# Performance work log

Measured on AMD Instinct MI355X. Metric: run time of the kernel, lower is better.

## Reference

```python
import jax, jax.numpy as jnp
import numpy as np

NUM_HEADS = 4
WINDOW_SIZE = 7
DILATION = 1


def local_mask(height, width, window_size, dilation):
    """[N, N] bool mask: True where token i may attend to token j (dilated 2D window)."""
    radius = window_size // 2
    rows = jnp.arange(height)
    cols = jnp.arange(width)
    r = jnp.repeat(rows, width)          # [N] row index of each flattened token
    c = jnp.tile(cols, height)           # [N] col index of each flattened token
    dr = r[:, None] - r[None, :]         # [N, N]
    dc = c[:, None] - c[None, :]
    within = (jnp.abs(dr) <= radius * dilation) & (jnpp_abs(dc) <= radius * dilation) if False else (
        (jnp.abs(dr) <= radius * dilation) & (jnp.abs(dc) <= radius * dilation)
    )
    on_grid = (dr % dilation == 0) & (dc % dilation == 0)
    return within & on_grid


def setup_inputs() -> dict:
    key = jax.random.key(0)
    kq, kk, kv = jax.random.split(key, 3)
    shape = (2, 64, 64, 64)  # (B, C, H, W)
    q = jax.random.normal(kq, shape, dtype=jnp.float32)
    k = jax.random.normal(kk, shape, dtype=jnp.float32)
    v = jax.random.normal(kv, shape, dtype=jnp.float32)
    return {"q": q, "k": k, "v": v}


def reference(q, k, v):
    B, C, H, W = q.shape
    nh = NUM_HEADS
    hd = C // nh
    N = H * W

    def to_seq(x):
        # (B, C, H, W) -> (B, nh, N, hd)
        x = x.reshape(B, nh, hd, H, W)
        return x.transpose(0, 1, 3, 4, 2).reshape(B, nh, N, hd)

    q_seq = to_seq(q)
    k_seq = to_seq(k)
    v_seq = to_seq(v)

    scale = 1.0 / jnp.sqrt(jnp.asarray(hd, dtype=q.dtype))
    scores = jnp.einsum("bhqd,bhkd->bhqk", q_seq, k_seq) * scale  # [B, nh, N, N]

    mask = local_mask(H, W, WINDOW_SIZE, DILATION)  # [N, N] bool
    neg = jnp.finfo(scores.dtype).min
    scores = jnp.where(mask[None, None, :, :], scores, neg)

    attn = jax.nn.softmax(scores, axis=-1)
    out = jnp.einsum("bhqk,bhkd->bhqd", attn, v_seq)  # [B, nh, N, hd]

    # (B, nh, N, hd) -> (B, C, H, W)
    out = out.reshape(B, nh, H, W, hd).transpose(0, 1, 4, 2, 3).reshape(B, C, H, W)
    return out
```

## Files before the change

kernel.cpp:

```cpp
#include <hip/hip_runtime.h>
#include <hip/hip_bf16.h>
#include <math.h>

#define HD  16
#define HW  4096
#define RAD 3

__device__ __forceinline__ float dpp_shl1(float x) {
#if defined(__has_builtin) && __has_builtin(__builtin_amdgcn_update_dpp)
    return __int_as_float(__builtin_amdgcn_update_dpp(
        0, __float_as_int(x), 0x130 , 0xf, 0xf, true));
#else
    int l = (int)(threadIdx.x & 63);
    return __shfl(x, l + 1, 64);
#endif
}
__device__ __forceinline__ float dpp_shr1(float x) {
#if defined(__has_builtin) && __has_builtin(__builtin_amdgcn_update_dpp)
    return __int_as_float(__builtin_amdgcn_update_dpp(
        0, __float_as_int(x), 0x138 , 0xf, 0xf, true));
#else
    int l = (int)(threadIdx.x & 63);
    return __shfl(x, l - 1, 64);
#endif
}

__global__ __launch_bounds__(512, 2)
void local_attn_kernel(const float* __restrict__ q,
                       const float* __restrict__ k,
                       const float* __restrict__ v,
                       float* __restrict__ out) {
    __shared__ float lds[18944];
    float* ldsK = lds;
    float* ldsV = lds + 8192;
    float* ldsQ = lds + 16384;

    const int tid = threadIdx.x;
    const int c   = tid & 63;
    const int w   = tid >> 6;

    const int bid = blockIdx.x;
    const int r0  = (bid & 31) * 2;
    const int h   = (bid >> 5) & 3;
    const int b   = bid >> 7;
    const int base = (b * 4 + h) * (HD * HW);

#pragma unroll
    for (int ii = 0; ii < 8; ++ii) {
        int ci = w * 8 + ii;
        int cj = ci & 31;
        const float* src = (ci < 32) ? (k + base) : (v + base);
        float* dst = (ci < 32) ? ldsK : ldsV;
        int s  = cj * 4 + (c >> 4);
        int d  = s >> 3;
        int hr = s & 7;
        int rr = r0 - RAD + hr;
        rr = rr < 0 ? 0 : (rr > 63 ? 63 : rr);
        const float* g = src + d * HW + rr * 64 + (c & 15) * 4;
#if defined(__has_builtin) && __has_builtin(__builtin_amdgcn_global_load_lds)
        __builtin_amdgcn_global_load_lds(
            (const __attribute__((address_space(1))) void*)g,
            (__attribute__((address_space(3))) void*)&dst[cj * 256], 16, 0, 0);
#else
        *(float4*)&dst[cj * 256 + c * 4] = *(const float4*)g;
#endif
    }

    {
        const int rq = w >> 2;
        const int dg = (w & 3) * 4;
        const int prow = (r0 + rq) * 64 + c;
#pragma unroll
        for (int i = 0; i < 4; ++i) {
            float x = q[base + (dg + i) * HW + prow] * 0.25f;
            ldsQ[(dg + i) * 128 + rq * 64 + c] = x;
        }
    }
    __syncthreads();

    const int  rr     = r0 - RAD + w;
    const bool rvalid = ((unsigned)rr < 64u);
    const bool do0    = rvalid && (w <= 6);
    const bool do1    = rvalid && (w >= 1);
    const int  lrow   = w * 64 + c;

    float s0[7], s1[7];
#pragma unroll
    for (int j = 0; j < 7; ++j) { s0[j] = 0.0f; s1[j] = 0.0f; }

#pragma unroll
    for (int d = 0; d < HD; ++d) {
        float kc  = ldsK[d * 512 + lrow];
        float a0  = ldsQ[d * 128 + c];
        float a1  = ldsQ[d * 128 + 64 + c];
        float kp1 = dpp_shl1(kc), kp2 = dpp_shl1(kp1), kp3 = dpp_shl1(kp2);
        float km1 = dpp_shr1(kc), km2 = dpp_shr1(km1), km3 = dpp_shr1(km2);
        s0[0] = fmaf(a0, km3, s0[0]);  s1[0] = fmaf(a1, km3, s1[0]);
        s0[1] = fmaf(a0, km2, s0[1]);  s1[1] = fmaf(a1, km2, s1[1]);
        s0[2] = fmaf(a0, km1, s0[2]);  s1[2] = fmaf(a1, km1, s1[2]);
        s0[3] = fmaf(a0, kc,  s0[3]);  s1[3] = fmaf(a1, kc,  s1[3]);
        s0[4] = fmaf(a0, kp1, s0[4]);  s1[4] = fmaf(a1, kp1, s1[4]);
        s0[5] = fmaf(a0, kp2, s0[5]);  s1[5] = fmaf(a1, kp2, s1[5]);
        s0[6] = fmaf(a0, kp3, s0[6]);  s1[6] = fmaf(a1, kp3, s1[6]);
    }

    float l0 = 0.0f, l1 = 0.0f;
#pragma unroll
    for (int j = 0; j < 7; ++j) {
        bool okc = ((unsigned)(c + j - RAD) < 64u);
        float p0 = (okc && do0) ? __expf(s0[j]) : 0.0f;
        float p1 = (okc && do1) ? __expf(s1[j]) : 0.0f;
        s0[j] = p0;  l0 += p0;
        s1[j] = p1;  l1 += p1;
    }

    float acc0[HD], acc1[HD];
#pragma unroll
    for (int d = 0; d < HD; ++d) {
        float vc  = ldsV[d * 512 + lrow];
        float vp1 = dpp_shl1(vc), vp2 = dpp_shl1(vp1), vp3 = dpp_shl1(vp2);
        float vm1 = dpp_shr1(vc), vm2 = dpp_shr1(vm1), vm3 = dpp_shr1(vm2);
        float a0, a1;
        a0 = s0[0] * vm3;            a1 = s1[0] * vm3;
        a0 = fmaf(s0[1], vm2, a0);   a1 = fmaf(s1[1], vm2, a1);
        a0 = fmaf(s0[2], vm1, a0);   a1 = fmaf(s1[2], vm1, a1);
        a0 = fmaf(s0[3], vc,  a0);   a1 = fmaf(s1[3], vc,  a1);
        a0 = fmaf(s0[4], vp1, a0);   a1 = fmaf(s1[4], vp1, a1);
        a0 = fmaf(s0[5], vp2, a0);   a1 = fmaf(s1[5], vp2, a1);
        a0 = fmaf(s0[6], vp3, a0);   a1 = fmaf(s1[6], vp3, a1);
        acc0[d] = a0;  acc1[d] = a1;
    }

    __syncthreads();

    const int bs = tid * 34;
#pragma unroll
    for (int d = 0; d < HD; d += 2) {
        *(float2*)&lds[bs + d]      = make_float2(acc0[d], acc0[d + 1]);
        *(float2*)&lds[bs + 16 + d] = make_float2(acc1[d], acc1[d + 1]);
    }
    *(float2*)&lds[bs + 32] = make_float2(l0, l1);
    __syncthreads();

    const int qq = w >> 2;
    const int dq = (w & 3) * 4;

    float lt = 0.0f;
#pragma unroll
    for (int s = 0; s < 8; ++s)
        lt += lds[(s * 64 + c) * 34 + 32 + qq];
    const float invl = 1.0f / lt;

    float a[4] = {0.0f, 0.0f, 0.0f, 0.0f};
#pragma unroll
    for (int s = 0; s < 8; ++s) {
        const int rb = (s * 64 + c) * 34 + qq * 16 + dq;
        float2 x0 = *(const float2*)&lds[rb];
        float2 x1 = *(const float2*)&lds[rb + 2];
        a[0] += x0.x;  a[1] += x0.y;  a[2] += x1.x;  a[3] += x1.y;
    }
#pragma unroll
    for (int i = 0; i < 4; ++i)
        out[base + (dq + i) * HW + (r0 + qq) * 64 + c] = a[i] * invl;
}

extern "C" void kernel_launch(void* const* d_in, const int* in_sizes, int n_in,
                              void* d_out, int out_size, void* d_ws, size_t ws_size,
                              hipStream_t stream) {
    const float* q = (const float*)d_in[0];
    const float* k = (const float*)d_in[1];
    const float* v = (const float*)d_in[2];
    float* out = (float*)d_out;

    int queries = out_size / HD;
    int blocks  = queries / 128;
    local_attn_kernel<<<blocks, 512, 0, stream>>>(q, k, v, out);
}
```

Measured before the change: 10.44 us.

## Process one query row per block with four waves covering seven key rows

```diff
diff --git a/kernel.cpp b/kernel.cpp
--- a/kernel.cpp
+++ b/kernel.cpp
@@ -25,36 +25,36 @@
 #endif
 }
 
-__global__ __launch_bounds__(512, 2)
+__global__ __launch_bounds__(256, 2)
 void local_attn_kernel(const float* __restrict__ q,
                        const float* __restrict__ k,
                        const float* __restrict__ v,
                        float* __restrict__ out) {
-    __shared__ float lds[18944];
+    __shared__ float lds[15360];
     float* ldsK = lds;
-    float* ldsV = lds + 8192;
-    float* ldsQ = lds + 16384;
+    float* ldsV = lds + 7168;
+    float* ldsQ = lds + 14336;
 
     const int tid = threadIdx.x;
     const int c   = tid & 63;
     const int w   = tid >> 6;
 
     const int bid = blockIdx.x;
-    const int r0  = (bid & 31) * 2;
-    const int h   = (bid >> 5) & 3;
-    const int b   = bid >> 7;
+    const int r   = bid & 63;
+    const int h   = (bid >> 6) & 3;
+    const int b   = bid >> 8;
     const int base = (b * 4 + h) * (HD * HW);
 
 #pragma unroll
-    for (int ii = 0; ii < 8; ++ii) {
-        int ci = w * 8 + ii;
-        int cj = ci & 31;
-        const float* src = (ci < 32) ? (k + base) : (v + base);
-        float* dst = (ci < 32) ? ldsK : ldsV;
+    for (int ii = 0; ii < 14; ++ii) {
+        int ci = w * 14 + ii;
+        int cj = (ci < 28) ? ci : ci - 28;
+        const float* src = (ci < 28) ? (k + base) : (v + base);
+        float* dst = (ci < 28) ? ldsK : ldsV;
         int s  = cj * 4 + (c >> 4);
-        int d  = s >> 3;
-        int hr = s & 7;
-        int rr = r0 - RAD + hr;
+        int d  = (int)((unsigned)s / 7u);
+        int hr = s - d * 7;
+        int rr = r - RAD + hr;
         rr = rr < 0 ? 0 : (rr > 63 ? 63 : rr);
         const float* g = src + d * HW + rr * 64 + (c & 15) * 4;
 #if defined(__has_builtin) && __has_builtin(__builtin_amdgcn_global_load_lds)
@@ -66,102 +66,98 @@
 #endif
     }
 
-    {
-        const int rq = w >> 2;
-        const int dg = (w & 3) * 4;
-        const int prow = (r0 + rq) * 64 + c;
 #pragma unroll
-        for (int i = 0; i < 4; ++i) {
-            float x = q[base + (dg + i) * HW + prow] * 0.25f;
-            ldsQ[(dg + i) * 128 + rq * 64 + c] = x;
-        }
+    for (int i = 0; i < 4; ++i) {
+        int d = w * 4 + i;
+        ldsQ[d * 64 + c] = q[base + d * HW + r * 64 + c] * 0.25f;
     }
     __syncthreads();
 
-    const int  rr     = r0 - RAD + w;
-    const bool rvalid = ((unsigned)rr < 64u);
-    const bool do0    = rvalid && (w <= 6);
-    const bool do1    = rvalid && (w >= 1);
-    const int  lrow   = w * 64 + c;
+    const int  hrA = w, hrB = w + 4;
+    const int  rrA = r - RAD + hrA;
+    const int  rrB = r - RAD + hrB;
+    const bool doA = ((unsigned)rrA < 64u);
+    const bool doB = (hrB < 7) && ((unsigned)rrB < 64u);
 
-    float s0[7], s1[7];
+    float sA[7], sB[7];
 #pragma unroll
-    for (int j = 0; j < 7; ++j) { s0[j] = 0.0f; s1[j] = 0.0f; }
+    for (int j = 0; j < 7; ++j) { sA[j] = 0.0f; sB[j] = 0.0f; }
 
 #pragma unroll
     for (int d = 0; d < HD; ++d) {
-        float kc  = ldsK[d * 512 + lrow];
-        float a0  = ldsQ[d * 128 + c];
-        float a1  = ldsQ[d * 128 + 64 + c];
-        float kp1 = dpp_shl1(kc), kp2 = dpp_shl1(kp1), kp3 = dpp_shl1(kp2);
-        float km1 = dpp_shr1(kc), km2 = dpp_shr1(km1), km3 = dpp_shr1(km2);
-        s0[0] = fmaf(a0, km3, s0[0]);  s1[0] = fmaf(a1, km3, s1[0]);
-        s0[1] = fmaf(a0, km2, s0[1]);  s1[1] = fmaf(a1, km2, s1[1]);
-        s0[2] = fmaf(a0, km1, s0[2]);  s1[2] = fmaf(a1, km1, s1[2]);
-        s0[3] = fmaf(a0, kc,  s0[3]);  s1[3] = fmaf(a1, kc,  s1[3]);
-        s0[4] = fmaf(a0, kp1, s0[4]);  s1[4] = fmaf(a1, kp1, s1[4]);
-        s0[5] = fmaf(a0, kp2, s0[5]);  s1[5] = fmaf(a1, kp2, s1[5]);
-        s0[6] = fmaf(a0, kp3, s0[6]);  s1[6] = fmaf(a1, kp3, s1[6]);
+        float qd = ldsQ[d * 64 + c];
+        float ka = ldsK[d * 448 + hrA * 64 + c];
+        float kb = ldsK[d * 448 + hrB * 64 + c];
+        float ap1 = dpp_shl1(ka), ap2 = dpp_shl1(ap1), ap3 = dpp_shl1(ap2);
+        float am1 = dpp_shr1(ka), am2 = dpp_shr1(am1), am3 = dpp_shr1(am2);
+        float bp1 = dpp_shl1(kb), bp2 = dpp_shl1(bp1), bp3 = dpp_shl1(bp2);
+        float bm1 = dpp_shr1(kb), bm2 = dpp_shr1(bm1), bm3 = dpp_shr1(bm2);
+        sA[0] = fmaf(qd, am3, sA[0]);  sB[0] = fmaf(qd, bm3, sB[0]);
+        sA[1] = fmaf(qd, am2, sA[1]);  sB[1] = fmaf(qd, bm2, sB[1]);
+        sA[2] = fmaf(qd, am1, sA[2]);  sB[2] = fmaf(qd, bm1, sB[2]);
+        sA[3] = fmaf(qd, ka,  sA[3]);  sB[3] = fmaf(qd, kb,  sB[3]);
+        sA[4] = fmaf(qd, ap1, sA[4]);  sB[4] = fmaf(qd, bp1, sB[4]);
+        sA[5] = fmaf(qd, ap2, sA[5]);  sB[5] = fmaf(qd, bp2, sB[5]);
+        sA[6] = fmaf(qd, ap3, sA[6]);  sB[6] = fmaf(qd, bp3, sB[6]);
     }
 
-    float l0 = 0.0f, l1 = 0.0f;
+    float lsum = 0.0f;
 #pragma unroll
     for (int j = 0; j < 7; ++j) {
         bool okc = ((unsigned)(c + j - RAD) < 64u);
-        float p0 = (okc && do0) ? __expf(s0[j]) : 0.0f;
-        float p1 = (okc && do1) ? __expf(s1[j]) : 0.0f;
-        s0[j] = p0;  l0 += p0;
-        s1[j] = p1;  l1 += p1;
+        float pA = (okc && doA) ? __expf(sA[j]) : 0.0f;
+        float pB = (okc && doB) ? __expf(sB[j]) : 0.0f;
+        sA[j] = pA;  sB[j] = pB;
+        lsum += pA + pB;
     }
 
-    float acc0[HD], acc1[HD];
+    float acc[HD];
 #pragma unroll
     for (int d = 0; d < HD; ++d) {
-        float vc  = ldsV[d * 512 + lrow];
-        float vp1 = dpp_shl1(vc), vp2 = dpp_shl1(vp1), vp3 = dpp_shl1(vp2);
-        float vm1 = dpp_shr1(vc), vm2 = dpp_shr1(vm1), vm3 = dpp_shr1(vm2);
-        float a0, a1;
-        a0 = s0[0] * vm3;            a1 = s1[0] * vm3;
-        a0 = fmaf(s0[1], vm2, a0);   a1 = fmaf(s1[1], vm2, a1);
-        a0 = fmaf(s0[2], vm1, a0);   a1 = fmaf(s1[2], vm1, a1);
-        a0 = fmaf(s0[3], vc,  a0);   a1 = fmaf(s1[3], vc,  a1);
-        a0 = fmaf(s0[4], vp1, a0);   a1 = fmaf(s1[4], vp1, a1);
-        a0 = fmaf(s0[5], vp2, a0);   a1 = fmaf(s1[5], vp2, a1);
-        a0 = fmaf(s0[6], vp3, a0);   a1 = fmaf(s1[6], vp3, a1);
-        acc0[d] = a0;  acc1[d] = a1;
+        float va = ldsV[d * 448 + hrA * 64 + c];
+        float vb = ldsV[d * 448 + hrB * 64 + c];
+        float ap1 = dpp_shl1(va), ap2 = dpp_shl1(ap1), ap3 = dpp_shl1(ap2);
+        float am1 = dpp_shr1(va), am2 = dpp_shr1(am1), am3 = dpp_shr1(am2);
+        float bp1 = dpp_shl1(vb), bp2 = dpp_shl1(bp1), bp3 = dpp_shl1(bp2);
+        float bm1 = dpp_shr1(vb), bm2 = dpp_shr1(bm1), bm3 = dpp_shr1(bm2);
+        float a;
+        a = sA[0] * am3;
+        a = fmaf(sA[1], am2, a);  a = fmaf(sA[2], am1, a);
+        a = fmaf(sA[3], va,  a);  a = fmaf(sA[4], ap1, a);
+        a = fmaf(sA[5], ap2, a);  a = fmaf(sA[6], ap3, a);
+        a = fmaf(sB[0], bm3, a);  a = fmaf(sB[1], bm2, a);
+        a = fmaf(sB[2], bm1, a);  a = fmaf(sB[3], vb,  a);
+        a = fmaf(sB[4], bp1, a);  a = fmaf(sB[5], bp2, a);
+        a = fmaf(sB[6], bp3, a);
+        acc[d] = a;
     }
 
     __syncthreads();
 
-    const int bs = tid * 34;
+    const int bs = tid * 18;
 #pragma unroll
-    for (int d = 0; d < HD; d += 2) {
-        *(float2*)&lds[bs + d]      = make_float2(acc0[d], acc0[d + 1]);
-        *(float2*)&lds[bs + 16 + d] = make_float2(acc1[d], acc1[d + 1]);
-    }
-    *(float2*)&lds[bs + 32] = make_float2(l0, l1);
+    for (int d = 0; d < HD; d += 2)
+        *(float2*)&lds[bs + d] = make_float2(acc[d], acc[d + 1]);
+    lds[bs + 16] = lsum;
     __syncthreads();
-
-    const int qq = w >> 2;
-    const int dq = (w & 3) * 4;
 
     float lt = 0.0f;
 #pragma unroll
-    for (int s = 0; s < 8; ++s)
-        lt += lds[(s * 64 + c) * 34 + 32 + qq];
+    for (int s = 0; s < 4; ++s)
+        lt += lds[(s * 64 + c) * 18 + 16];
     const float invl = 1.0f / lt;
 
     float a[4] = {0.0f, 0.0f, 0.0f, 0.0f};
 #pragma unroll
-    for (int s = 0; s < 8; ++s) {
-        const int rb = (s * 64 + c) * 34 + qq * 16 + dq;
+    for (int s = 0; s < 4; ++s) {
+        const int rb = (s * 64 + c) * 18 + w * 4;
         float2 x0 = *(const float2*)&lds[rb];
         float2 x1 = *(const float2*)&lds[rb + 2];
         a[0] += x0.x;  a[1] += x0.y;  a[2] += x1.x;  a[3] += x1.y;
     }
 #pragma unroll
     for (int i = 0; i < 4; ++i)
-        out[base + (dq + i) * HW + (r0 + qq) * 64 + c] = a[i] * invl;
+        out[base + (w * 4 + i) * HW + r * 64 + c] = a[i] * invl;
 }
 
 extern "C" void kernel_launch(void* const* d_in, const int* in_sizes, int n_in,
@@ -173,6 +169,6 @@
     float* out = (float*)d_out;
 
     int queries = out_size / HD;
-    int blocks  = queries / 128;
-    local_attn_kernel<<<blocks, 512, 0, stream>>>(q, k, v, out);
+    int blocks  = queries / 64;
+    local_attn_kernel<<<blocks, 256, 0, stream>>>(q, k, v, out);
 }
```

Result: slower. 11.32 us (+8.4%).
